# Kernel tuning notes

Measured on AMD Instinct MI355X. Metric: run time of the kernel, lower is better.

The kernel has to match this reference:

```python
import jax, jax.numpy as jnp
import numpy as np

N_NODES = 50000
HEADS = 3
C = 64  # node_channels
NEG_SLOPE = 0.2


def setup_inputs() -> dict:
    key = jax.random.key(0)
    ks = jax.random.split(key, 8)
    E = 800000
    x = jax.random.normal(ks[0], (N_NODES, C), dtype=jnp.float32)
    edge_index = jax.random.randint(ks[1], (2, E), 0, N_NODES, dtype=jnp.int64)
    edge_attr = jax.random.normal(ks[2], (E, 16), dtype=jnp.float32)
    weight_node = jax.random.normal(ks[3], (C, HEADS * C), dtype=jnp.float32) * 0.1
    weight_edge = jax.random.normal(ks[4], (16, HEADS * C), dtype=jnp.float32) * 0.1
    weight_triplet_att = jax.random.normal(ks[5], (1, HEADS, 3 * C), dtype=jnp.float32) * 0.1
    weight_scale = jax.random.normal(ks[6], (HEADS * C, C), dtype=jnp.float32) * 0.1
    bias = jnp.zeros((C,), dtype=jnp.float32)
    return {"x": x, "edge_index": edge_index, "edge_attr": edge_attr,
            "weight_node": weight_node, "weight_edge": weight_edge,
            "weight_triplet_att": weight_triplet_att,
            "weight_scale": weight_scale, "bias": bias}


def reference(x, edge_index, edge_attr, weight_node, weight_edge,
              weight_triplet_att, weight_scale, bias):
    E = edge_index.shape[1]
    src = edge_index[0]  # j (source)
    dst = edge_index[1]  # i (target, softmax/aggregation index)

    x_proj = x @ weight_node              # [N, H*C]
    e = edge_attr @ weight_edge           # [E, H*C]

    x_j = x_proj[src].reshape(E, HEADS, C)
    x_i = x_proj[dst].reshape(E, HEADS, C)
    e_ij = e.reshape(E, HEADS, C)

    # attention weights split over the triplet concat [x_i | e_ij | x_j]
    w = weight_triplet_att.reshape(HEADS, 3, C)  # [H,3,C]
    alpha = (jnp.einsum('ehc,hc->eh', x_i, w[:, 0])
             + jnp.einsum('ehc,hc->eh', e_ij, w[:, 1])
             + jnp.einsum('ehc,hc->eh', x_j, w[:, 2]))  # [E,H]
    alpha = jnp.where(alpha >= 0, alpha, NEG_SLOPE * alpha)  # leaky_relu

    # scatter-softmax over incoming edges of each target node
    m = jax.ops.segment_max(alpha, dst, num_segments=N_NODES)  # [N,H]
    m = jnp.where(jnp.isfinite(m), m, 0.0)
    exp_a = jnp.exp(alpha - m[dst])
    denom = jax.ops.segment_sum(exp_a, dst, num_segments=N_NODES)  # [N,H]
    alpha = exp_a / (denom[dst] + 1e-16)

    msg = alpha[:, :, None] * e_ij * x_j  # [E,H,C]
    aggr = jax.ops.segment_sum(msg.reshape(E, HEADS * C), dst,
                               num_segments=N_NODES)  # [N,H*C]
    return aggr @ weight_scale + bias
```

## Files before the change

kernel.cpp:

```cpp
#include <hip/hip_runtime.h>
#include <hip/hip_bf16.h>


#define N_NODES 50000
#define CCH 64
#define HEADS 3
#define HC 192
#define NEG_SLOPE 0.2f
#define NWAVES 12288
#define NBX 3125
#define NSCAN 49

typedef _Float16 h2 __attribute__((ext_vector_type(2)));
__device__ __forceinline__ h2 uh(unsigned u) {
    union { unsigned u; h2 h; } x; x.u = u; return x.h;
}
__device__ __forceinline__ unsigned hu(float a, float b) {
    union { unsigned u; _Float16 h[2]; } x;
    x.h[0] = (_Float16)a; x.h[1] = (_Float16)b; return x.u;
}

__device__ __forceinline__ void gbar(int* bar, int phase, int nb) {
    __syncthreads();
    if (threadIdx.x == 0) {
        __threadfence();
        __hip_atomic_fetch_add(&bar[phase], 1, __ATOMIC_ACQ_REL,
                               __HIP_MEMORY_SCOPE_AGENT);
        while (__hip_atomic_load(&bar[phase], __ATOMIC_ACQUIRE,
                                 __HIP_MEMORY_SCOPE_AGENT) < nb) {}
        __threadfence();
    }
    __syncthreads();
}

__global__ __launch_bounds__(192) void k_front(
    const float* __restrict__ x, const float* __restrict__ Wn,
    const float* __restrict__ Watt, uint2* __restrict__ xph2,
    float* __restrict__ a0, float* __restrict__ a2,
    const int* __restrict__ ei, int* __restrict__ cnt,
    const float* __restrict__ We, float* __restrict__ v1, int E) {
    int t = threadIdx.x;
    int bx = blockIdx.x;
    if (bx >= NBX) {
        int e = (bx - NBX) * 192 + t;
        if (e < E) atomicAdd(&cnt[ei[E + e]], 1);
        if (bx == NBX && t < HEADS * 16) {
            int h = t / 16, k = t % 16;
            float s = 0.f;
            #pragma unroll
            for (int c = 0; c < CCH; ++c)
                s = fmaf(We[k * HC + h * CCH + c], Watt[h * HC + CCH + c], s);
            v1[t] = s;
        }
        return;
    }
    __shared__ _Float16 pack[16 * CCH * 4];
    float wreg[CCH];
    #pragma unroll
    for (int k = 0; k < CCH; ++k) wreg[k] = Wn[k * HC + t];
    int base = bx * 16;
    int h = t >> 6, c = t & 63;
    float w0 = Watt[h * HC + c];
    float w2 = Watt[h * HC + 2 * CCH + c];
    int jmax = N_NODES - base; jmax = jmax > 16 ? 16 : jmax;
    #pragma unroll 1
    for (int j = 0; j < jmax; ++j) {
        const float* xr = x + (size_t)(base + j) * CCH;
        float val = 0.f;
        #pragma unroll
        for (int k = 0; k < CCH; ++k) val = fmaf(xr[k], wreg[k], val);
        pack[(j * CCH + c) * 4 + h] = (_Float16)val;
        if (h == 0) pack[(j * CCH + c) * 4 + 3] = (_Float16)0.f;
        float p0 = val * w0, p2 = val * w2;
        #pragma unroll
        for (int off = 32; off; off >>= 1) {
            p0 += __shfl_down(p0, off);
            p2 += __shfl_down(p2, off);
        }
        if (c == 0) {
            a0[(base + j) * HEADS + h] = p0;
            a2[(base + j) * HEADS + h] = p2;
        }
    }
    __syncthreads();
    const uint2* p2v = (const uint2*)pack;
    for (int i = t; i < 16 * CCH; i += 192) {
        int n = base + (i >> 6);
        if (n < N_NODES) xph2[(size_t)base * CCH + i] = p2v[i];
    }
}

__global__ __launch_bounds__(1024) void k_scan49(
    const int* __restrict__ cnt, int* __restrict__ off, int* __restrict__ cursor,
    int* __restrict__ wstart, int* __restrict__ bar, int* __restrict__ bsum,
    int E) {
    __shared__ int ws[16];
    __shared__ int bof_s;
    int b = blockIdx.x, t = threadIdx.x, lane = t & 63, wid = t >> 6;
    int i = b * 1024 + t;
    int v = (i < N_NODES) ? cnt[i] : 0;
    {
        int r = v;
        #pragma unroll
        for (int o = 32; o; o >>= 1) r += __shfl_down(r, o);
        if (lane == 0) ws[wid] = r;
        __syncthreads();
        if (wid == 0) {
            int s = (lane < 16) ? ws[lane] : 0;
            #pragma unroll
            for (int o = 8; o; o >>= 1) s += __shfl_down(s, o);
            if (lane == 0) bsum[b] = s;
        }
    }
    gbar(bar, 0, NSCAN);
    int x = v;
    #pragma unroll
    for (int o = 1; o < 64; o <<= 1) {
        int y = __shfl_up(x, o);
        if (lane >= o) x += y;
    }
    if (lane == 63) ws[wid] = x;
    __syncthreads();
    if (wid == 0) {
        int s = (lane < 16) ? ws[lane] : 0;
        #pragma unroll
        for (int o = 1; o < 16; o <<= 1) {
            int y = __shfl_up(s, o);
            if (lane >= o) s += y;
        }
        if (lane < 16) ws[lane] = s;
    } else if (wid == 1) {
        int bv = (lane < NSCAN) ? bsum[lane] : 0;
        int bx = bv;
        #pragma unroll
        for (int o = 1; o < 64; o <<= 1) {
            int y = __shfl_up(bx, o);
            if (lane >= o) bx += y;
        }
        if (lane == b) bof_s = bx - bv;
    }
    __syncthreads();
    int excl = bof_s + (wid ? ws[wid - 1] : 0) + x - v;
    if (i < N_NODES) { off[i] = excl; cursor[i] = excl; }
    if (b == 0 && t == 0) off[N_NODES] = E;
    gbar(bar, 1, NSCAN);
    int w = i;
    if (w <= NWAVES) {
        if (w == NWAVES) { wstart[NWAVES] = N_NODES; }
        else {
            long tgt = (long)E * w / NWAVES;
            int lo = 0, hi = N_NODES;
            while (lo < hi) {
                int mid = (lo + hi) >> 1;
                if (off[mid] < (int)tgt) lo = mid + 1; else hi = mid;
            }
            wstart[w] = lo;
        }
    }
}

__global__ __launch_bounds__(256) void k_place(
    const int* __restrict__ ei, const float* __restrict__ ea,
    const float* __restrict__ a0, const float* __restrict__ a2,
    const float* __restrict__ v1, int* __restrict__ cursor,
    float* __restrict__ recs, int E) {
    int e = blockIdx.x * 256 + threadIdx.x;
    if (e >= E) return;
    int src = ei[e], dst = ei[E + e];
    const float4* q = (const float4*)(ea + (size_t)e * 16);
    float4 q0 = q[0], q1 = q[1], q2 = q[2], q3 = q[3];
    float at[16] = {q0.x, q0.y, q0.z, q0.w, q1.x, q1.y, q1.z, q1.w,
                    q2.x, q2.y, q2.z, q2.w, q3.x, q3.y, q3.z, q3.w};
    float ex[HEADS];
    #pragma unroll
    for (int h = 0; h < HEADS; ++h) {
        float s = a0[dst * HEADS + h] + a2[src * HEADS + h];
        #pragma unroll
        for (int j = 0; j < 16; ++j) s = fmaf(at[j], v1[h * 16 + j], s);
        s = (s >= 0.f) ? s : NEG_SLOPE * s;
        ex[h] = __expf(s);
    }
    int pos = atomicAdd(&cursor[dst], 1);
    float* rp = recs + (size_t)pos * 12;
    uint4 r0 = {hu(at[0], at[1]), hu(at[2], at[3]), hu(at[4], at[5]), hu(at[6], at[7])};
    uint4 r1 = {hu(at[8], at[9]), hu(at[10], at[11]), hu(at[12], at[13]), hu(at[14], at[15])};
    float4 r2 = {ex[0], ex[1], ex[2], __int_as_float(src)};
    *(uint4*)rp = r0;
    *(uint4*)(rp + 4) = r1;
    *(float4*)(rp + 8) = r2;
}

__global__ __launch_bounds__(256, 6) void k_msg(
    const int* __restrict__ off, const int* __restrict__ wstart,
    const float* __restrict__ recs, const uint2* __restrict__ xph2,
    const float* __restrict__ We, _Float16* __restrict__ rowsH) {
    int lane = threadIdx.x & 63;
    int w = blockIdx.x * 4 + (threadIdx.x >> 6);
    #define WP(h, q) hu(We[(2*(q)) * HC + (h) * CCH + lane], \
                        We[(2*(q)+1) * HC + (h) * CCH + lane])
    unsigned w00 = WP(0,0), w01 = WP(0,1), w02 = WP(0,2), w03 = WP(0,3),
             w04 = WP(0,4), w05 = WP(0,5), w06 = WP(0,6), w07 = WP(0,7);
    unsigned w10 = WP(1,0), w11 = WP(1,1), w12 = WP(1,2), w13 = WP(1,3),
             w14 = WP(1,4), w15 = WP(1,5), w16 = WP(1,6), w17 = WP(1,7);
    unsigned w20 = WP(2,0), w21 = WP(2,1), w22 = WP(2,2), w23 = WP(2,3),
             w24 = WP(2,4), w25 = WP(2,5), w26 = WP(2,6), w27 = WP(2,7);
    #undef WP

    int n0 = wstart[w], n1 = wstart[w + 1];
    n0 = __builtin_amdgcn_readfirstlane(n0);
    n1 = __builtin_amdgcn_readfirstlane(n1);
    if (n0 >= n1) return;

    int n = n0;
    int k    = __builtin_amdgcn_readfirstlane(off[n0]);
    int kend = __builtin_amdgcn_readfirstlane(off[n1]);
    int re   = __builtin_amdgcn_readfirstlane(off[n0 + 1]);

    float acc0 = 0.f, acc1 = 0.f, acc2 = 0.f;
    float den0 = 0.f, den1 = 0.f, den2 = 0.f;

    uint4 U0, U1; float4 RX; uint2 xv;
    if (k < kend) {
        const float* rp = recs + (size_t)k * 12;
        U0 = *(const uint4*)rp;
        U1 = *(const uint4*)(rp + 4);
        RX = *(const float4*)(rp + 8);
        int src = __builtin_amdgcn_readfirstlane(__float_as_int(RX.w));
        xv = xph2[(size_t)src * CCH + lane];
    }

    #define FLUSH(nn)                                                      \
        {                                                                  \
            size_t ro = (size_t)(nn) * HC + lane;                          \
            rowsH[ro]           = (_Float16)(acc0 / (den0 + 1e-16f));      \
            rowsH[ro + CCH]     = (_Float16)(acc1 / (den1 + 1e-16f));      \
            rowsH[ro + 2 * CCH] = (_Float16)(acc2 / (den2 + 1e-16f));      \
            acc0 = acc1 = acc2 = den0 = den1 = den2 = 0.f;                 \
        }

    while (k < kend) {
        while (k == re) {
            FLUSH(n);
            ++n;
            re = __builtin_amdgcn_readfirstlane(off[n + 1]);
        }
        int kn = (k + 1 < kend) ? k + 1 : k;
        const float* rpn = recs + (size_t)kn * 12;
        uint4 U0n = *(const uint4*)rpn;
        uint4 U1n = *(const uint4*)(rpn + 4);
        float4 RXn = *(const float4*)(rpn + 8);
        float ev0 = 0.f, ev1 = 0.f, ev2 = 0.f;
        #define D(u, wv, acc) acc = __builtin_amdgcn_fdot2(uh(u), uh(wv), acc, false);
        D(U0.x, w00, ev0) D(U0.x, w10, ev1) D(U0.x, w20, ev2)
        D(U0.y, w01, ev0) D(U0.y, w11, ev1) D(U0.y, w21, ev2)
        D(U0.z, w02, ev0) D(U0.z, w12, ev1) D(U0.z, w22, ev2)
        D(U0.w, w03, ev0) D(U0.w, w13, ev1) D(U0.w, w23, ev2)
        D(U1.x, w04, ev0) D(U1.x, w14, ev1) D(U1.x, w24, ev2)
        D(U1.y, w05, ev0) D(U1.y, w15, ev1) D(U1.y, w25, ev2)
        D(U1.z, w06, ev0) D(U1.z, w16, ev1) D(U1.z, w26, ev2)
        D(U1.w, w07, ev0) D(U1.w, w17, ev1) D(U1.w, w27, ev2)
        #undef D
        h2 xa = uh(xv.x), xb = uh(xv.y);
        den0 += RX.x; den1 += RX.y; den2 += RX.z;
        acc0 = fmaf(RX.x * ev0, (float)xa.x, acc0);
        acc1 = fmaf(RX.y * ev1, (float)xa.y, acc1);
        acc2 = fmaf(RX.z * ev2, (float)xb.x, acc2);
        U0 = U0n; U1 = U1n; RX = RXn;
        int src_n = __builtin_amdgcn_readfirstlane(__float_as_int(RXn.w));
        xv = xph2[(size_t)src_n * CCH + lane];
        ++k;
    }
    FLUSH(n);
    while (++n < n1) FLUSH(n);
    #undef FLUSH
}

__global__ __launch_bounds__(256) void k_out(
    const _Float16* __restrict__ rowsH, const float* __restrict__ Ws,
    const float* __restrict__ bias, float* __restrict__ out) {
    int lane = threadIdx.x & 63;
    int wgid = __builtin_amdgcn_readfirstlane(blockIdx.x * 4 + (threadIdx.x >> 6));
    float b = bias[lane];
    #define WQ(q) hu(Ws[(2*(q)) * CCH + lane], Ws[(2*(q)+1) * CCH + lane])
    unsigned s00=WQ(0),  s01=WQ(1),  s02=WQ(2),  s03=WQ(3),  s04=WQ(4),  s05=WQ(5),  s06=WQ(6),  s07=WQ(7);
    unsigned s08=WQ(8),  s09=WQ(9),  s10=WQ(10), s11=WQ(11), s12=WQ(12), s13=WQ(13), s14=WQ(14), s15=WQ(15);
    unsigned s16=WQ(16), s17=WQ(17), s18=WQ(18), s19=WQ(19), s20=WQ(20), s21=WQ(21), s22=WQ(22), s23=WQ(23);
    unsigned s24=WQ(24), s25=WQ(25), s26=WQ(26), s27=WQ(27), s28=WQ(28), s29=WQ(29), s30=WQ(30), s31=WQ(31);
    unsigned s32=WQ(32), s33=WQ(33), s34=WQ(34), s35=WQ(35), s36=WQ(36), s37=WQ(37), s38=WQ(38), s39=WQ(39);
    unsigned s40=WQ(40), s41=WQ(41), s42=WQ(42), s43=WQ(43), s44=WQ(44), s45=WQ(45), s46=WQ(46), s47=WQ(47);
    unsigned s48=WQ(48), s49=WQ(49), s50=WQ(50), s51=WQ(51), s52=WQ(52), s53=WQ(53), s54=WQ(54), s55=WQ(55);
    unsigned s56=WQ(56), s57=WQ(57), s58=WQ(58), s59=WQ(59), s60=WQ(60), s61=WQ(61), s62=WQ(62), s63=WQ(63);
    unsigned s64=WQ(64), s65=WQ(65), s66=WQ(66), s67=WQ(67), s68=WQ(68), s69=WQ(69), s70=WQ(70), s71=WQ(71);
    unsigned s72=WQ(72), s73=WQ(73), s74=WQ(74), s75=WQ(75), s76=WQ(76), s77=WQ(77), s78=WQ(78), s79=WQ(79);
    unsigned s80=WQ(80), s81=WQ(81), s82=WQ(82), s83=WQ(83), s84=WQ(84), s85=WQ(85), s86=WQ(86), s87=WQ(87);
    unsigned s88=WQ(88), s89=WQ(89), s90=WQ(90), s91=WQ(91), s92=WQ(92), s93=WQ(93), s94=WQ(94), s95=WQ(95);
    #undef WQ
    #pragma unroll 1
    for (int n = wgid; n < N_NODES; n += 1024) {
        const unsigned* rp = (const unsigned*)(rowsH + (size_t)n * HC);
        float a0_ = b, a1_ = 0.f, a2_ = 0.f, a3_ = 0.f;
        #define DQ(q, sreg, acc) acc = __builtin_amdgcn_fdot2(uh(rp[q]), uh(sreg), acc, false);
        DQ(0,s00,a0_)  DQ(1,s01,a1_)  DQ(2,s02,a2_)  DQ(3,s03,a3_)
        DQ(4,s04,a0_)  DQ(5,s05,a1_)  DQ(6,s06,a2_)  DQ(7,s07,a3_)
        DQ(8,s08,a0_)  DQ(9,s09,a1_)  DQ(10,s10,a2_) DQ(11,s11,a3_)
        DQ(12,s12,a0_) DQ(13,s13,a1_) DQ(14,s14,a2_) DQ(15,s15,a3_)
        DQ(16,s16,a0_) DQ(17,s17,a1_) DQ(18,s18,a2_) DQ(19,s19,a3_)
        DQ(20,s20,a0_) DQ(21,s21,a1_) DQ(22,s22,a2_) DQ(23,s23,a3_)
        DQ(24,s24,a0_) DQ(25,s25,a1_) DQ(26,s26,a2_) DQ(27,s27,a3_)
        DQ(28,s28,a0_) DQ(29,s29,a1_) DQ(30,s30,a2_) DQ(31,s31,a3_)
        DQ(32,s32,a0_) DQ(33,s33,a1_) DQ(34,s34,a2_) DQ(35,s35,a3_)
        DQ(36,s36,a0_) DQ(37,s37,a1_) DQ(38,s38,a2_) DQ(39,s39,a3_)
        DQ(40,s40,a0_) DQ(41,s41,a1_) DQ(42,s42,a2_) DQ(43,s43,a3_)
        DQ(44,s44,a0_) DQ(45,s45,a1_) DQ(46,s46,a2_) DQ(47,s47,a3_)
        DQ(48,s48,a0_) DQ(49,s49,a1_) DQ(50,s50,a2_) DQ(51,s51,a3_)
        DQ(52,s52,a0_) DQ(53,s53,a1_) DQ(54,s54,a2_) DQ(55,s55,a3_)
        DQ(56,s56,a0_) DQ(57,s57,a1_) DQ(58,s58,a2_) DQ(59,s59,a3_)
        DQ(60,s60,a0_) DQ(61,s61,a1_) DQ(62,s62,a2_) DQ(63,s63,a3_)
        DQ(64,s64,a0_) DQ(65,s65,a1_) DQ(66,s66,a2_) DQ(67,s67,a3_)
        DQ(68,s68,a0_) DQ(69,s69,a1_) DQ(70,s70,a2_) DQ(71,s71,a3_)
        DQ(72,s72,a0_) DQ(73,s73,a1_) DQ(74,s74,a2_) DQ(75,s75,a3_)
        DQ(76,s76,a0_) DQ(77,s77,a1_) DQ(78,s78,a2_) DQ(79,s79,a3_)
        DQ(80,s80,a0_) DQ(81,s81,a1_) DQ(82,s82,a2_) DQ(83,s83,a3_)
        DQ(84,s84,a0_) DQ(85,s85,a1_) DQ(86,s86,a2_) DQ(87,s87,a3_)
        DQ(88,s88,a0_) DQ(89,s89,a1_) DQ(90,s90,a2_) DQ(91,s91,a3_)
        DQ(92,s92,a0_) DQ(93,s93,a1_) DQ(94,s94,a2_) DQ(95,s95,a3_)
        #undef DQ
        out[(size_t)n * CCH + lane] = (a0_ + a1_) + (a2_ + a3_);
    }
}

extern "C" void kernel_launch(void* const* d_in, const int* in_sizes, int n_in,
                              void* d_out, int out_size, void* d_ws, size_t ws_size,
                              hipStream_t stream) {
    const float* x    = (const float*)d_in[0];
    const int*   ei   = (const int*)d_in[1];
    const float* ea   = (const float*)d_in[2];
    const float* Wn   = (const float*)d_in[3];
    const float* We   = (const float*)d_in[4];
    const float* Watt = (const float*)d_in[5];
    const float* Ws   = (const float*)d_in[6];
    const float* bias = (const float*)d_in[7];
    float* out = (float*)d_out;

    const int E = in_sizes[1] / 2;

    char* w = (char*)d_ws;
    size_t o = 0;
    int*   cnt    = (int*)(w + o);    o += 50048 * 4;
    int*   bar    = (int*)(w + o);    o += 16 * 4;
    int*   off    = (int*)(w + o);    o += 50064 * 4;
    int*   cursor = (int*)(w + o);    o += 50048 * 4;
    int*   wst    = (int*)(w + o);    o += (NWAVES + 16) * 4;
    int*   bsum   = (int*)(w + o);    o += 64 * 4;
    float* v1     = (float*)(w + o);  o += 64 * 4;
    float* a0     = (float*)(w + o);  o += 150016 * 4;
    float* a2     = (float*)(w + o);  o += 150016 * 4;
    uint2* xph2   = (uint2*)(w + o);  o += (size_t)N_NODES * CCH * 8;
    _Float16* rowsH = (_Float16*)(w + o); o += (size_t)N_NODES * HC * 2;
    float* recs   = (float*)(w + o);  o += (size_t)E * 48;

    hipMemsetAsync(cnt, 0, (50048 + 16) * 4, stream);

    const int nbh = (E + 191) / 192;
    k_front<<<NBX + nbh, 192, 0, stream>>>(x, Wn, Watt, xph2, a0, a2,
                                           ei, cnt, We, v1, E);
    k_scan49<<<NSCAN, 1024, 0, stream>>>(cnt, off, cursor, wst, bar, bsum, E);
    k_place<<<(E + 255) / 256, 256, 0, stream>>>(ei, ea, a0, a2, v1, cursor, recs, E);
    k_msg<<<NWAVES / 4, 256, 0, stream>>>(off, wst, recs, xph2, We, rowsH);
    k_out<<<256, 256, 0, stream>>>(rowsH, Ws, bias, out);
}
```

Before: 372.1 us.

## Deepen k_msg edge prefetch to two records and widen k_out grid

The per-edge loop in k_msg now keeps two edge records and their gathered source features in flight instead of one, so the x gather for edge k+2 is issued while edge k is computed. This is meant to hide more of the latency of the dependent record-then-gather loads. The output projection kernel now uses a grid-derived stride and launches 768 blocks instead of 256, giving more waves to cover row loads. The cost is extra VGPRs in k_msg, which may lower occupancy, and more redundant weight-register setup in k_out.

```diff
diff --git a/kernel.cpp b/kernel.cpp
--- a/kernel.cpp
+++ b/kernel.cpp
@@ -219,14 +219,21 @@
     float acc0 = 0.f, acc1 = 0.f, acc2 = 0.f;
     float den0 = 0.f, den1 = 0.f, den2 = 0.f;
 
-    uint4 U0, U1; float4 RX; uint2 xv;
+    uint4 U0a, U1a, U0b, U1b; float4 RXa, RXb; uint2 xva, xvb;
     if (k < kend) {
         const float* rp = recs + (size_t)k * 12;
-        U0 = *(const uint4*)rp;
-        U1 = *(const uint4*)(rp + 4);
-        RX = *(const float4*)(rp + 8);
-        int src = __builtin_amdgcn_readfirstlane(__float_as_int(RX.w));
-        xv = xph2[(size_t)src * CCH + lane];
+        U0a = *(const uint4*)rp;
+        U1a = *(const uint4*)(rp + 4);
+        RXa = *(const float4*)(rp + 8);
+        int s0 = __builtin_amdgcn_readfirstlane(__float_as_int(RXa.w));
+        xva = xph2[(size_t)s0 * CCH + lane];
+        int k1 = (k + 1 < kend) ? k + 1 : k;
+        const float* rq = recs + (size_t)k1 * 12;
+        U0b = *(const uint4*)rq;
+        U1b = *(const uint4*)(rq + 4);
+        RXb = *(const float4*)(rq + 8);
+        int s1 = __builtin_amdgcn_readfirstlane(__float_as_int(RXb.w));
+        xvb = xph2[(size_t)s1 * CCH + lane];
     }
 
     #define FLUSH(nn)                                                      \
@@ -244,30 +251,31 @@
             ++n;
             re = __builtin_amdgcn_readfirstlane(off[n + 1]);
         }
-        int kn = (k + 1 < kend) ? k + 1 : k;
-        const float* rpn = recs + (size_t)kn * 12;
+        int k2 = (k + 2 < kend) ? k + 2 : kend - 1;
+        const float* rpn = recs + (size_t)k2 * 12;
         uint4 U0n = *(const uint4*)rpn;
         uint4 U1n = *(const uint4*)(rpn + 4);
         float4 RXn = *(const float4*)(rpn + 8);
         float ev0 = 0.f, ev1 = 0.f, ev2 = 0.f;
         #define D(u, wv, acc) acc = __builtin_amdgcn_fdot2(uh(u), uh(wv), acc, false);
-        D(U0.x, w00, ev0) D(U0.x, w10, ev1) D(U0.x, w20, ev2)
-        D(U0.y, w01, ev0) D(U0.y, w11, ev1) D(U0.y, w21, ev2)
-        D(U0.z, w02, ev0) D(U0.z, w12, ev1) D(U0.z, w22, ev2)
-        D(U0.w, w03, ev0) D(U0.w, w13, ev1) D(U0.w, w23, ev2)
-        D(U1.x, w04, ev0) D(U1.x, w14, ev1) D(U1.x, w24, ev2)
-        D(U1.y, w05, ev0) D(U1.y, w15, ev1) D(U1.y, w25, ev2)
-        D(U1.z, w06, ev0) D(U1.z, w16, ev1) D(U1.z, w26, ev2)
-        D(U1.w, w07, ev0) D(U1.w, w17, ev1) D(U1.w, w27, ev2)
+        D(U0a.x, w00, ev0) D(U0a.x, w10, ev1) D(U0a.x, w20, ev2)
+        D(U0a.y, w01, ev0) D(U0a.y, w11, ev1) D(U0a.y, w21, ev2)
+        D(U0a.z, w02, ev0) D(U0a.z, w12, ev1) D(U0a.z, w22, ev2)
+        D(U0a.w, w03, ev0) D(U0a.w, w13, ev1) D(U0a.w, w23, ev2)
+        D(U1a.x, w04, ev0) D(U1a.x, w14, ev1) D(U1a.x, w24, ev2)
+        D(U1a.y, w05, ev0) D(U1a.y, w15, ev1) D(U1a.y, w25, ev2)
+        D(U1a.z, w06, ev0) D(U1a.z, w16, ev1) D(U1a.z, w26, ev2)
+        D(U1a.w, w07, ev0) D(U1a.w, w17, ev1) D(U1a.w, w27, ev2)
         #undef D
-        h2 xa = uh(xv.x), xb = uh(xv.y);
-        den0 += RX.x; den1 += RX.y; den2 += RX.z;
-        acc0 = fmaf(RX.x * ev0, (float)xa.x, acc0);
-        acc1 = fmaf(RX.y * ev1, (float)xa.y, acc1);
-        acc2 = fmaf(RX.z * ev2, (float)xb.x, acc2);
-        U0 = U0n; U1 = U1n; RX = RXn;
-        int src_n = __builtin_amdgcn_readfirstlane(__float_as_int(RXn.w));
-        xv = xph2[(size_t)src_n * CCH + lane];
+        h2 xa = uh(xva.x), xb = uh(xva.y);
+        den0 += RXa.x; den1 += RXa.y; den2 += RXa.z;
+        acc0 = fmaf(RXa.x * ev0, (float)xa.x, acc0);
+        acc1 = fmaf(RXa.y * ev1, (float)xa.y, acc1);
+        acc2 = fmaf(RXa.z * ev2, (float)xb.x, acc2);
+        U0a = U0b; U1a = U1b; RXa = RXb; xva = xvb;
+        U0b = U0n; U1b = U1n; RXb = RXn;
+        int s2 = __builtin_amdgcn_readfirstlane(__float_as_int(RXn.w));
+        xvb = xph2[(size_t)s2 * CCH + lane];
         ++k;
     }
     FLUSH(n);
@@ -280,6 +288,7 @@
     const float* __restrict__ bias, float* __restrict__ out) {
     int lane = threadIdx.x & 63;
     int wgid = __builtin_amdgcn_readfirstlane(blockIdx.x * 4 + (threadIdx.x >> 6));
+    int stride = (int)gridDim.x * 4;
     float b = bias[lane];
     #define WQ(q) hu(Ws[(2*(q)) * CCH + lane], Ws[(2*(q)+1) * CCH + lane])
     unsigned s00=WQ(0),  s01=WQ(1),  s02=WQ(2),  s03=WQ(3),  s04=WQ(4),  s05=WQ(5),  s06=WQ(6),  s07=WQ(7);
@@ -296,7 +305,7 @@
     unsigned s88=WQ(88), s89=WQ(89), s90=WQ(90), s91=WQ(91), s92=WQ(92), s93=WQ(93), s94=WQ(94), s95=WQ(95);
     #undef WQ
     #pragma unroll 1
-    for (int n = wgid; n < N_NODES; n += 1024) {
+    for (int n = wgid; n < N_NODES; n += stride) {
         const unsigned* rp = (const unsigned*)(rowsH + (size_t)n * HC);
         float a0_ = b, a1_ = 0.f, a2_ = 0.f, a3_ = 0.f;
         #define DQ(q, sreg, acc) acc = __builtin_amdgcn_fdot2(uh(rp[q]), uh(sreg), acc, false);
@@ -367,5 +376,5 @@
     k_scan49<<<NSCAN, 1024, 0, stream>>>(cnt, off, cursor, wst, bar, bsum, E);
     k_place<<<(E + 255) / 256, 256, 0, stream>>>(ei, ea, a0, a2, v1, cursor, recs, E);
     k_msg<<<NWAVES / 4, 256, 0, stream>>>(off, wst, recs, xph2, We, rowsH);
-    k_out<<<256, 256, 0, stream>>>(rowsH, Ws, bias, out);
-}
+    k_out<<<768, 256, 0, stream>>>(rowsH, Ws, bias, out);
+}
```

Result: faster. 362.8 us (-2.5%).
